# Performance work log

Measured on AMD Instinct MI355X. Metric: run time of the kernel, lower is better.

Reference implementation:

```python
import jax, jax.numpy as jnp
import numpy as np

D_MODEL = 1024
HEADS = 16
D_K = D_MODEL // HEADS

def setup_inputs() -> dict:
    key = jax.random.key(0)
    ks = jax.random.split(key, 12)
    B, S = 4, 2048
    sc = 1.0 / np.sqrt(D_MODEL)
    inp = {
        'q': jax.random.normal(ks[0], (B, S, D_MODEL), jnp.float32),
        'k': jax.random.normal(ks[1], (B, S, D_MODEL), jnp.float32),
        'v': jax.random.normal(ks[2], (B, S, D_MODEL), jnp.float32),
        'mask': jnp.ones((B, S, S), jnp.int32),
        'Wq': jax.random.normal(ks[3], (D_MODEL, D_MODEL), jnp.float32) * sc,
        'bq': jnp.zeros((D_MODEL,), jnp.float32),
        'Wk': jax.random.normal(ks[4], (D_MODEL, D_MODEL), jnp.float32) * sc,
        'bk': jnp.zeros((D_MODEL,), jnp.float32),
        'Wv': jax.random.normal(ks[5], (D_MODEL, D_MODEL), jnp.float32) * sc,
        'bv': jnp.zeros((D_MODEL,), jnp.float32),
        'Wo': jax.random.normal(ks[6], (D_MODEL, D_MODEL), jnp.float32) * sc,
        'bo': jnp.zeros((D_MODEL,), jnp.float32),
    }
    return inp

def _proj_heads(x, W, b):
    # torch Linear: y = x @ W.T + b; then view(B,S,h,dk).transpose(1,2) -> [B,h,S,dk]
    B, S, _ = x.shape
    y = jnp.einsum('bsd,ed->bse', x, W) + b
    return y.reshape(B, S, HEADS, D_K).transpose(0, 2, 1, 3)

def reference(q, k, v, mask, Wq, bq, Wk, bk, Wv, bv, Wo, bo):
    B, S, _ = q.shape
    qh = _proj_heads(q, Wq, bq)  # [B,h,S,dk]
    kh = _proj_heads(k, Wk, bk)
    vh = _proj_heads(v, Wv, bv)
    scores = jnp.einsum('bhqd,bhkd->bhqk', qh, kh) / np.sqrt(D_K)
    scores = jnp.where(mask[:, None, :, :] == 0, jnp.float32(-1e9), scores)
    probs = jax.nn.softmax(scores, axis=-1)  # dropout = identity (eval mode)
    ctx = jnp.einsum('bhqk,bhkd->bhqd', probs, vh)
    concat = ctx.transpose(0, 2, 1, 3).reshape(B, S, D_MODEL)
    return jnp.einsum('bsd,ed->bse', concat, Wo) + bo
```

## Files before the change

### kernel.cpp

```cpp
#include <hip/hip_runtime.h>
#include <stdint.h>

#define DM 1024
#define SQL 2048
#define NB 4
#define NH 16
#define DK 64

typedef unsigned short u16;
typedef unsigned int u32;
typedef float f32x4 __attribute__((ext_vector_type(4)));
typedef short s16x8 __attribute__((ext_vector_type(8)));

__device__ __forceinline__ u16 f2bf(float x) {
  union { float f; u32 u; } un; un.f = x;
  u32 r = un.u + 0x7fffu + ((un.u >> 16) & 1u);
  return (u16)(r >> 16);
}
__device__ __forceinline__ u32 pack_bf16(float a, float b) {
  return (u32)f2bf(a) | ((u32)f2bf(b) << 16);
}

typedef __attribute__((address_space(3))) u32 lds_u32_t;
typedef __attribute__((address_space(1))) u32 g_u32_t;

__device__ __forceinline__ void async_cp16(void* lds, const void* g) {
  __builtin_amdgcn_global_load_lds((g_u32_t*)(unsigned long long)g,
                                   (lds_u32_t*)(unsigned long long)lds,
                                   16, 0, 0);
}

__device__ __forceinline__ void mfma16(f32x4& c, s16x8 a, s16x8 b) {
  c = __builtin_amdgcn_mfma_f32_16x16x32_bf16(a, b, c, 0, 0, 0);
}

__global__ void init_flag_k(int* flag) { if (threadIdx.x == 0) *flag = 1; }

__device__ __forceinline__ void store_bf4(u16* dst, float4 v) {
  u32 lo = pack_bf16(v.x, v.y);
  u32 hi = pack_bf16(v.z, v.w);
  ((u32*)dst)[0] = lo; ((u32*)dst)[1] = hi;
}

__global__ void __launch_bounds__(256) convert_scan_k(
    const float* __restrict__ q, const float* __restrict__ k, const float* __restrict__ v,
    const float* __restrict__ wq, const float* __restrict__ wk,
    const float* __restrict__ wv, const float* __restrict__ wo,
    const int* __restrict__ mask,
    u16* qb, u16* kb, u16* vb, u16* wqb, u16* wkb, u16* wvb, u16* wob, int* flag)
{
  const size_t i = (size_t)blockIdx.x * 256 + threadIdx.x;
  const size_t i4 = i * 4;
  store_bf4(qb + i4, *(const float4*)(q + i4));
  store_bf4(kb + i4, *(const float4*)(k + i4));
  store_bf4(vb + i4, *(const float4*)(v + i4));
  if (i4 < 1048576) {
    store_bf4(wqb + i4, *(const float4*)(wq + i4));
    store_bf4(wkb + i4, *(const float4*)(wk + i4));
    store_bf4(wvb + i4, *(const float4*)(wv + i4));
    store_bf4(wob + i4, *(const float4*)(wo + i4));
  }
  const size_t mi = i * 8;
  int4 m0 = *(const int4*)(mask + mi);
  int4 m1 = *(const int4*)(mask + mi + 4);
  bool z = (m0.x == 0) | (m0.y == 0) | (m0.z == 0) | (m0.w == 0) |
           (m1.x == 0) | (m1.y == 0) | (m1.z == 0) | (m1.w == 0);
  if (z) *flag = 0;
}

__device__ __forceinline__ void gemm_core(const u16* __restrict__ A, const u16* __restrict__ W,
                                          int m0, int n0, u16* sA, u16* sB, f32x4 (&acc)[4][4])
{
  const int tid = threadIdx.x;
  const int l = tid & 63, w = tid >> 6;
  const int g = l >> 4, ln = l & 15;
  const int wm = w & 1, wn = w >> 1;

  for (int kt = 0; kt < DM; kt += 64) {
#pragma unroll
    for (int i = 0; i < 4; ++i) {
      int s = w * 256 + i * 64 + l;
      int m = s >> 3;
      int kc = (s & 7) ^ (m & 7);
      async_cp16(sA + (size_t)(w * 256 + i * 64) * 8,
                 A + (size_t)(m0 + m) * DM + kt + kc * 8);
    }
#pragma unroll
    for (int i = 0; i < 4; ++i) {
      int s = w * 256 + i * 64 + l;
      int n = s >> 3;
      int kc = (s & 7) ^ (n & 7);
      async_cp16(sB + (size_t)(w * 256 + i * 64) * 8,
                 W + (size_t)(n0 + n) * DM + kt + kc * 8);
    }
    asm volatile("s_waitcnt vmcnt(0)" ::: "memory");
    __syncthreads();
#pragma unroll
    for (int ks = 0; ks < 2; ++ks) {
      s16x8 af[4], bfr[4];
#pragma unroll
      for (int mt = 0; mt < 4; ++mt) {
        int m = wm * 64 + mt * 16 + ln;
        int slot = m * 8 + ((ks * 4 + g) ^ (m & 7));
        af[mt] = *(const s16x8*)(sA + (size_t)slot * 8);
      }
#pragma unroll
      for (int nt = 0; nt < 4; ++nt) {
        int n = wn * 64 + nt * 16 + ln;
        int slot = n * 8 + ((ks * 4 + g) ^ (n & 7));
        bfr[nt] = *(const s16x8*)(sB + (size_t)slot * 8);
      }
#pragma unroll
      for (int mt = 0; mt < 4; ++mt)
#pragma unroll
        for (int nt = 0; nt < 4; ++nt)
          mfma16(acc[mt][nt], af[mt], bfr[nt]);
    }
    __syncthreads();
  }
}

__global__ void __launch_bounds__(256) gemm_qkv_k(
    const u16* __restrict__ qb, const u16* __restrict__ kb, const u16* __restrict__ vb,
    const u16* __restrict__ wqb, const u16* __restrict__ wkb, const u16* __restrict__ wvb,
    const float* __restrict__ bq, const float* __restrict__ bk, const float* __restrict__ bv,
    u16* Qh, u16* Kh, u16* Vt)
{
  __shared__ __align__(16) u16 sA[128 * 64];
  __shared__ __align__(16) u16 sB[128 * 64];
  const int z = blockIdx.z;
  const u16* A = (z == 0) ? qb : ((z == 1) ? kb : vb);
  const u16* W = (z == 0) ? wqb : ((z == 1) ? wkb : wvb);
  const float* bias = (z == 0) ? bq : ((z == 1) ? bk : bv);
  const int m0 = blockIdx.y * 128, n0 = blockIdx.x * 128;

  f32x4 zero4 = {0.f, 0.f, 0.f, 0.f};
  f32x4 acc[4][4];
#pragma unroll
  for (int mt = 0; mt < 4; ++mt)
#pragma unroll
    for (int nt = 0; nt < 4; ++nt) acc[mt][nt] = zero4;

  gemm_core(A, W, m0, n0, sA, sB, acc);

  const int tid = threadIdx.x;
  const int l = tid & 63, w = tid >> 6, g = l >> 4, ln = l & 15;
  const int wm = w & 1, wn = w >> 1;
  const float scale = (z == 0) ? (0.125f * 1.44269504089f) : 1.0f;
  u16* Crow = (z == 0) ? Qh : Kh;
#pragma unroll
  for (int nt = 0; nt < 4; ++nt) {
    int n = n0 + wn * 64 + nt * 16 + ln;
    float bn = bias[n];
#pragma unroll
    for (int mt = 0; mt < 4; ++mt) {
      int mb = m0 + wm * 64 + mt * 16 + g * 4;
      f32x4 vv = acc[mt][nt];
      if (z < 2) {
#pragma unroll
        for (int r = 0; r < 4; ++r)
          Crow[(size_t)(mb + r) * DM + n] = f2bf((vv[r] + bn) * scale);
      } else {
        int b = mb >> 11, s = mb & 2047;
        u32 lo = pack_bf16(vv[0] + bn, vv[1] + bn);
        u32 hi = pack_bf16(vv[2] + bn, vv[3] + bn);
        u32* dst = (u32*)(Vt + ((size_t)b << 21) + (size_t)n * SQL + s);
        dst[0] = lo; dst[1] = hi;
      }
    }
  }
}

__global__ void __launch_bounds__(256, 4) attn_k(
    const u16* __restrict__ Qh, const u16* __restrict__ Kh, const u16* __restrict__ Vt,
    const int* __restrict__ mask, const int* __restrict__ flag, u16* __restrict__ ctx)
{
  __shared__ __align__(16) u16 smem[16384];
  u16* Ks = smem;
  u16* Vs = smem + 8192;
  const int tid = threadIdx.x;
  const int l = tid & 63, w = tid >> 6, g = l >> 4, ln = l & 15;
  const int wq = w >> 1, wk = w & 1;
  const int q0 = blockIdx.x * 64;
  const int h = blockIdx.y, b = blockIdx.z;
  const int allones = *flag;

  s16x8 qf[2][2];
#pragma unroll
  for (int u = 0; u < 2; ++u)
#pragma unroll
    for (int ks = 0; ks < 2; ++ks) {
      size_t row = (size_t)(b * SQL + q0 + wq * 32 + u * 16 + ln);
      qf[u][ks] = *(const s16x8*)(Qh + row * DM + h * DK + ks * 32 + g * 8);
    }

  f32x4 zero4 = {0.f, 0.f, 0.f, 0.f};
  f32x4 ot[4][2];
#pragma unroll
  for (int mt = 0; mt < 4; ++mt) { ot[mt][0] = zero4; ot[mt][1] = zero4; }
  float lsum[2] = {0.f, 0.f};

  const int LA = (g & 1) * 32 + ln;
  const int LB = LA + 16;
  const bool ghi = (g >> 1) != 0;

  for (int kv0 = 0; kv0 < SQL; kv0 += 128) {
#pragma unroll
    for (int i = 0; i < 4; ++i) {
      int s = w * 256 + i * 64 + l;
      int m = s >> 3;
      int kc = (s & 7) ^ (m & 7);
      async_cp16(Ks + (size_t)(w * 256 + i * 64) * 8,
                 Kh + (size_t)(b * SQL + kv0 + m) * DM + h * DK + kc * 8);
    }
#pragma unroll
    for (int i = 0; i < 4; ++i) {
      int s = w * 256 + i * 64 + l;
      int d = s >> 4;
      int kc = (s & 15) ^ (d & 15);
      async_cp16(Vs + (size_t)(w * 256 + i * 64) * 8,
                 Vt + ((size_t)b << 21) + (size_t)(h * DK + d) * SQL + kv0 + kc * 8);
    }
    asm volatile("s_waitcnt vmcnt(0)" ::: "memory");
    __syncthreads();

    f32x4 st[4][2];
#pragma unroll
    for (int t = 0; t < 4; ++t) { st[t][0] = zero4; st[t][1] = zero4; }
#pragma unroll
    for (int ks = 0; ks < 2; ++ks) {
#pragma unroll
      for (int t = 0; t < 4; ++t) {
        int m = wk * 64 + t * 16 + ln;
        int slot = m * 8 + ((ks * 4 + g) ^ (m & 7));
        s16x8 kf = *(const s16x8*)(Ks + (size_t)slot * 8);
        mfma16(st[t][0], kf, qf[0][ks]);
        mfma16(st[t][1], kf, qf[1][ks]);
      }
    }

    if (!allones) {
      const int* mb_ = mask + (size_t)b * SQL * SQL;
#pragma unroll
      for (int t = 0; t < 4; ++t)
#pragma unroll
        for (int u = 0; u < 2; ++u)
#pragma unroll
          for (int r = 0; r < 4; ++r) {
            int kv = kv0 + wk * 64 + t * 16 + g * 4 + r;
            int qq = q0 + wq * 32 + u * 16 + ln;
            if (mb_[(size_t)qq * SQL + kv] == 0) st[t][u][r] = -30.f;
          }
    }

    u32 pk[2][4][2];
#pragma unroll
    for (int u = 0; u < 2; ++u) {
      float rs = 0.f;
#pragma unroll
      for (int t = 0; t < 4; ++t) {
        float p0 = __builtin_amdgcn_exp2f(st[t][u][0]);
        float p1 = __builtin_amdgcn_exp2f(st[t][u][1]);
        float p2 = __builtin_amdgcn_exp2f(st[t][u][2]);
        float p3 = __builtin_amdgcn_exp2f(st[t][u][3]);
        rs += (p0 + p1) + (p2 + p3);
        pk[u][t][0] = pack_bf16(p0, p1);
        pk[u][t][1] = pack_bf16(p2, p3);
      }
      rs += __shfl_xor(rs, 16, 64);
      rs += __shfl_xor(rs, 32, 64);
      lsum[u] += rs;
    }

#pragma unroll
    for (int kc = 0; kc < 2; ++kc) {
      s16x8 pf[2];
#pragma unroll
      for (int u = 0; u < 2; ++u) {
        u32 a0 = __shfl(pk[u][kc * 2][0], LA, 64);
        u32 a1 = __shfl(pk[u][kc * 2][1], LA, 64);
        u32 b0 = __shfl(pk[u][kc * 2][0], LB, 64);
        u32 b1 = __shfl(pk[u][kc * 2][1], LB, 64);
        u32 c0 = __shfl(pk[u][kc * 2 + 1][0], LA, 64);
        u32 c1 = __shfl(pk[u][kc * 2 + 1][1], LA, 64);
        u32 d0 = __shfl(pk[u][kc * 2 + 1][0], LB, 64);
        u32 d1 = __shfl(pk[u][kc * 2 + 1][1], LB, 64);
        union { u32 wds[4]; s16x8 v; } pu;
        pu.wds[0] = ghi ? c0 : a0;
        pu.wds[1] = ghi ? c1 : a1;
        pu.wds[2] = ghi ? d0 : b0;
        pu.wds[3] = ghi ? d1 : b1;
        pf[u] = pu.v;
      }
#pragma unroll
      for (int mt = 0; mt < 4; ++mt) {
        int d = mt * 16 + ln;
        int slot = d * 16 + ((wk * 8 + kc * 4 + g) ^ (d & 15));
        s16x8 vf = *(const s16x8*)(Vs + (size_t)slot * 8);
        mfma16(ot[mt][0], vf, pf[0]);
        mfma16(ot[mt][1], vf, pf[1]);
      }
    }
    __syncthreads();
  }

  float* red = (float*)smem;
  if (wk == 1) {
#pragma unroll
    for (int u = 0; u < 2; ++u) {
      int row = wq * 32 + u * 16 + ln;
#pragma unroll
      for (int mt = 0; mt < 4; ++mt)
        *(f32x4*)&red[(size_t)row * 68 + mt * 16 + g * 4] = ot[mt][u];
      if (g == 0) red[(size_t)row * 68 + 64] = lsum[u];
    }
  }
  __syncthreads();
  if (wk == 0) {
#pragma unroll
    for (int u = 0; u < 2; ++u) {
      int row = wq * 32 + u * 16 + ln;
#pragma unroll
      for (int mt = 0; mt < 4; ++mt)
        ot[mt][u] += *(const f32x4*)&red[(size_t)row * 68 + mt * 16 + g * 4];
      lsum[u] += red[(size_t)row * 68 + 64];
    }
#pragma unroll
    for (int u = 0; u < 2; ++u) {
      float inv = 1.0f / lsum[u];
      size_t row = (size_t)(b * SQL + q0 + wq * 32 + u * 16 + ln);
#pragma unroll
      for (int mt = 0; mt < 4; ++mt) {
        u32 lo = pack_bf16(ot[mt][u][0] * inv, ot[mt][u][1] * inv);
        u32 hi = pack_bf16(ot[mt][u][2] * inv, ot[mt][u][3] * inv);
        u32* dst = (u32*)(ctx + row * DM + h * DK + mt * 16 + g * 4);
        dst[0] = lo; dst[1] = hi;
      }
    }
  }
}

__global__ void __launch_bounds__(256) gemm_out_k(
    const u16* __restrict__ ctx, const u16* __restrict__ wob,
    const float* __restrict__ bo, float* __restrict__ out)
{
  __shared__ __align__(16) u16 sA[128 * 64];
  __shared__ __align__(16) u16 sB[128 * 64];
  const int m0 = blockIdx.y * 128, n0 = blockIdx.x * 128;
  f32x4 zero4 = {0.f, 0.f, 0.f, 0.f};
  f32x4 acc[4][4];
#pragma unroll
  for (int mt = 0; mt < 4; ++mt)
#pragma unroll
    for (int nt = 0; nt < 4; ++nt) acc[mt][nt] = zero4;

  gemm_core(ctx, wob, m0, n0, sA, sB, acc);

  const int tid = threadIdx.x;
  const int l = tid & 63, w = tid >> 6, g = l >> 4, ln = l & 15;
  const int wm = w & 1, wn = w >> 1;
#pragma unroll
  for (int nt = 0; nt < 4; ++nt) {
    int n = n0 + wn * 64 + nt * 16 + ln;
    float bn = bo[n];
#pragma unroll
    for (int mt = 0; mt < 4; ++mt) {
      int mb = m0 + wm * 64 + mt * 16 + g * 4;
      f32x4 vv = acc[mt][nt];
#pragma unroll
      for (int r = 0; r < 4; ++r)
        out[(size_t)(mb + r) * DM + n] = vv[r] + bn;
    }
  }
}

extern "C" void kernel_launch(void* const* d_in, const int* in_sizes, int n_in,
                              void* d_out, int out_size, void* d_ws, size_t ws_size,
                              hipStream_t stream) {
  (void)in_sizes; (void)n_in; (void)out_size; (void)ws_size;
  const float* q  = (const float*)d_in[0];
  const float* k  = (const float*)d_in[1];
  const float* v  = (const float*)d_in[2];
  const int* mask = (const int*)d_in[3];
  const float* Wq = (const float*)d_in[4];
  const float* bq = (const float*)d_in[5];
  const float* Wk = (const float*)d_in[6];
  const float* bk = (const float*)d_in[7];
  const float* Wv = (const float*)d_in[8];
  const float* bv = (const float*)d_in[9];
  const float* Wo = (const float*)d_in[10];
  const float* bo = (const float*)d_in[11];
  float* out = (float*)d_out;
  char* ws = (char*)d_ws;

  u16* qb  = (u16*)(ws + 0);
  u16* kb  = (u16*)(ws + 16777216);
  u16* vb  = (u16*)(ws + 33554432);
  u16* Qh  = (u16*)(ws + 50331648);
  u16* Kh  = (u16*)(ws + 67108864);
  u16* Vt  = (u16*)(ws + 83886080);
  u16* ctx = (u16*)(ws + 100663296);
  u16* wqb = (u16*)(ws + 117440512);
  u16* wkb = (u16*)(ws + 119537664);
  u16* wvb = (u16*)(ws + 121634816);
  u16* wob = (u16*)(ws + 123731968);
  int* flag = (int*)(ws + 125829120);

  hipLaunchKernelGGL(init_flag_k, dim3(1), dim3(64), 0, stream, flag);
  hipLaunchKernelGGL(convert_scan_k, dim3(8192), dim3(256), 0, stream,
                     q, k, v, Wq, Wk, Wv, Wo, mask,
                     qb, kb, vb, wqb, wkb, wvb, wob, flag);
  hipLaunchKernelGGL(gemm_qkv_k, dim3(8, 64, 3), dim3(256), 0, stream,
                     qb, kb, vb, wqb, wkb, wvb, bq, bk, bv, Qh, Kh, Vt);
  hipLaunchKernelGGL(attn_k, dim3(32, 16, 4), dim3(256), 0, stream,
                     Qh, Kh, Vt, mask, flag, ctx);
  hipLaunchKernelGGL(gemm_out_k, dim3(8, 64), dim3(256), 0, stream,
                     ctx, wob, bo, out);
}
```

Baseline: 472.3 us.

## Double-buffer K/V staging in attention and remap blocks for locality

The attention kernel now prefetches the next 128-key K/V tile into a second LDS buffer while computing the current one, waiting with partial vmcnt and raw s_barrier. Block indices are remapped so that neighbouring blocks spread across batch/head groups, the row-sum shuffle reduction moves out of the loop, and the epilogue stages normalized output through LDS for coalesced bf16 stores. bf16 rounding is simplified from round-to-nearest-even to round-half-up. LDS doubles and the occupancy hint drops from 4 to 2 blocks, trading occupancy for overlap of loads and compute.

```diff
diff --git a/kernel.cpp b/kernel.cpp
--- a/kernel.cpp
+++ b/kernel.cpp
@@ -14,8 +14,7 @@
 
 __device__ __forceinline__ u16 f2bf(float x) {
   union { float f; u32 u; } un; un.f = x;
-  u32 r = un.u + 0x7fffu + ((un.u >> 16) & 1u);
-  return (u16)(r >> 16);
+  return (u16)((un.u + 0x8000u) >> 16);
 }
 __device__ __forceinline__ u32 pack_bf16(float a, float b) {
   return (u32)f2bf(a) | ((u32)f2bf(b) << 16);
@@ -171,18 +170,41 @@
   }
 }
 
-__global__ void __launch_bounds__(256, 4) attn_k(
+__device__ __forceinline__ void stage_kv(u16* Ks, u16* Vs,
+                                         const u16* __restrict__ Kh,
+                                         const u16* __restrict__ Vt,
+                                         int b, int h, int kv0, int w, int l) {
+#pragma unroll
+  for (int i = 0; i < 4; ++i) {
+    int s = w * 256 + i * 64 + l;
+    int m = s >> 3;
+    int kc = (s & 7) ^ (m & 7);
+    async_cp16(Ks + (size_t)(w * 256 + i * 64) * 8,
+               Kh + (size_t)(b * SQL + kv0 + m) * DM + h * DK + kc * 8);
+  }
+#pragma unroll
+  for (int i = 0; i < 4; ++i) {
+    int s = w * 256 + i * 64 + l;
+    int d = s >> 4;
+    int kc = (s & 15) ^ (d & 15);
+    async_cp16(Vs + (size_t)(w * 256 + i * 64) * 8,
+               Vt + ((size_t)b << 21) + (size_t)(h * DK + d) * SQL + kv0 + kc * 8);
+  }
+}
+
+__global__ void __launch_bounds__(256, 2) attn_k(
     const u16* __restrict__ Qh, const u16* __restrict__ Kh, const u16* __restrict__ Vt,
     const int* __restrict__ mask, const int* __restrict__ flag, u16* __restrict__ ctx)
 {
-  __shared__ __align__(16) u16 smem[16384];
-  u16* Ks = smem;
-  u16* Vs = smem + 8192;
+  __shared__ __align__(16) u16 smem[32768];
   const int tid = threadIdx.x;
   const int l = tid & 63, w = tid >> 6, g = l >> 4, ln = l & 15;
   const int wq = w >> 1, wk = w & 1;
-  const int q0 = blockIdx.x * 64;
-  const int h = blockIdx.y, b = blockIdx.z;
+  const int flat = blockIdx.x + 32 * (blockIdx.y + 16 * blockIdx.z);
+  const int nid = (flat & 7) * 256 + (flat >> 3);
+  const int q0 = (nid & 31) * 64;
+  const int bh = nid >> 5;
+  const int h = bh & 15, b = bh >> 4;
   const int allones = *flag;
 
   s16x8 qf[2][2];
@@ -204,72 +226,63 @@
   const int LB = LA + 16;
   const bool ghi = (g >> 1) != 0;
 
-  for (int kv0 = 0; kv0 < SQL; kv0 += 128) {
-#pragma unroll
-    for (int i = 0; i < 4; ++i) {
-      int s = w * 256 + i * 64 + l;
-      int m = s >> 3;
-      int kc = (s & 7) ^ (m & 7);
-      async_cp16(Ks + (size_t)(w * 256 + i * 64) * 8,
-                 Kh + (size_t)(b * SQL + kv0 + m) * DM + h * DK + kc * 8);
-    }
-#pragma unroll
-    for (int i = 0; i < 4; ++i) {
-      int s = w * 256 + i * 64 + l;
-      int d = s >> 4;
-      int kc = (s & 15) ^ (d & 15);
-      async_cp16(Vs + (size_t)(w * 256 + i * 64) * 8,
-                 Vt + ((size_t)b << 21) + (size_t)(h * DK + d) * SQL + kv0 + kc * 8);
-    }
-    asm volatile("s_waitcnt vmcnt(0)" ::: "memory");
-    __syncthreads();
+  stage_kv(smem, smem + 8192, Kh, Vt, b, h, 0, w, l);
+
+  for (int t = 0; t < 16; ++t) {
+    const int kv0 = t * 128;
+    u16* Ks = smem + (t & 1) * 16384;
+    u16* Vs = smem + 8192 + (t & 1) * 16384;
+    if (t < 15) {
+      stage_kv(smem + ((t + 1) & 1) * 16384, smem + 8192 + ((t + 1) & 1) * 16384,
+               Kh, Vt, b, h, kv0 + 128, w, l);
+      asm volatile("s_waitcnt vmcnt(8)" ::: "memory");
+    } else {
+      asm volatile("s_waitcnt vmcnt(0)" ::: "memory");
+    }
+    asm volatile("s_barrier" ::: "memory");
 
     f32x4 st[4][2];
 #pragma unroll
-    for (int t = 0; t < 4; ++t) { st[t][0] = zero4; st[t][1] = zero4; }
+    for (int t2 = 0; t2 < 4; ++t2) { st[t2][0] = zero4; st[t2][1] = zero4; }
 #pragma unroll
     for (int ks = 0; ks < 2; ++ks) {
 #pragma unroll
-      for (int t = 0; t < 4; ++t) {
-        int m = wk * 64 + t * 16 + ln;
+      for (int t2 = 0; t2 < 4; ++t2) {
+        int m = wk * 64 + t2 * 16 + ln;
         int slot = m * 8 + ((ks * 4 + g) ^ (m & 7));
         s16x8 kf = *(const s16x8*)(Ks + (size_t)slot * 8);
-        mfma16(st[t][0], kf, qf[0][ks]);
-        mfma16(st[t][1], kf, qf[1][ks]);
+        mfma16(st[t2][0], kf, qf[0][ks]);
+        mfma16(st[t2][1], kf, qf[1][ks]);
       }
     }
 
     if (!allones) {
       const int* mb_ = mask + (size_t)b * SQL * SQL;
 #pragma unroll
-      for (int t = 0; t < 4; ++t)
+      for (int t2 = 0; t2 < 4; ++t2)
 #pragma unroll
         for (int u = 0; u < 2; ++u)
 #pragma unroll
           for (int r = 0; r < 4; ++r) {
-            int kv = kv0 + wk * 64 + t * 16 + g * 4 + r;
+            int kv = kv0 + wk * 64 + t2 * 16 + g * 4 + r;
             int qq = q0 + wq * 32 + u * 16 + ln;
-            if (mb_[(size_t)qq * SQL + kv] == 0) st[t][u][r] = -30.f;
+            if (mb_[(size_t)qq * SQL + kv] == 0) st[t2][u][r] = -30.f;
           }
     }
 
     u32 pk[2][4][2];
 #pragma unroll
     for (int u = 0; u < 2; ++u) {
-      float rs = 0.f;
-#pragma unroll
-      for (int t = 0; t < 4; ++t) {
-        float p0 = __builtin_amdgcn_exp2f(st[t][u][0]);
-        float p1 = __builtin_amdgcn_exp2f(st[t][u][1]);
-        float p2 = __builtin_amdgcn_exp2f(st[t][u][2]);
-        float p3 = __builtin_amdgcn_exp2f(st[t][u][3]);
-        rs += (p0 + p1) + (p2 + p3);
-        pk[u][t][0] = pack_bf16(p0, p1);
-        pk[u][t][1] = pack_bf16(p2, p3);
-      }
-      rs += __shfl_xor(rs, 16, 64);
-      rs += __shfl_xor(rs, 32, 64);
-      lsum[u] += rs;
+#pragma unroll
+      for (int t2 = 0; t2 < 4; ++t2) {
+        float p0 = __builtin_amdgcn_exp2f(st[t2][u][0]);
+        float p1 = __builtin_amdgcn_exp2f(st[t2][u][1]);
+        float p2 = __builtin_amdgcn_exp2f(st[t2][u][2]);
+        float p3 = __builtin_amdgcn_exp2f(st[t2][u][3]);
+        lsum[u] += (p0 + p1) + (p2 + p3);
+        pk[u][t2][0] = pack_bf16(p0, p1);
+        pk[u][t2][1] = pack_bf16(p2, p3);
+      }
     }
 
 #pragma unroll
@@ -301,10 +314,19 @@
         mfma16(ot[mt][1], vf, pf[1]);
       }
     }
-    __syncthreads();
+
+    asm volatile("s_waitcnt lgkmcnt(0)" ::: "memory");
+    asm volatile("s_barrier" ::: "memory");
+  }
+
+#pragma unroll
+  for (int u = 0; u < 2; ++u) {
+    lsum[u] += __shfl_xor(lsum[u], 16, 64);
+    lsum[u] += __shfl_xor(lsum[u], 32, 64);
   }
 
   float* red = (float*)smem;
+  __syncthreads();
   if (wk == 1) {
 #pragma unroll
     for (int u = 0; u < 2; ++u) {
@@ -325,18 +347,28 @@
         ot[mt][u] += *(const f32x4*)&red[(size_t)row * 68 + mt * 16 + g * 4];
       lsum[u] += red[(size_t)row * 68 + 64];
     }
+  }
+  __syncthreads();
+  if (wk == 0) {
 #pragma unroll
     for (int u = 0; u < 2; ++u) {
       float inv = 1.0f / lsum[u];
-      size_t row = (size_t)(b * SQL + q0 + wq * 32 + u * 16 + ln);
-#pragma unroll
-      for (int mt = 0; mt < 4; ++mt) {
-        u32 lo = pack_bf16(ot[mt][u][0] * inv, ot[mt][u][1] * inv);
-        u32 hi = pack_bf16(ot[mt][u][2] * inv, ot[mt][u][3] * inv);
-        u32* dst = (u32*)(ctx + row * DM + h * DK + mt * 16 + g * 4);
-        dst[0] = lo; dst[1] = hi;
-      }
-    }
+      int row = wq * 32 + u * 16 + ln;
+#pragma unroll
+      for (int mt = 0; mt < 4; ++mt)
+#pragma unroll
+        for (int r = 0; r < 4; ++r)
+          red[(size_t)row * 68 + mt * 16 + g * 4 + r] = ot[mt][u][r] * inv;
+    }
+  }
+  __syncthreads();
+#pragma unroll
+  for (int i = 0; i < 8; ++i) {
+    int f2 = i * 256 + tid;
+    int qq = f2 >> 5, dp = f2 & 31;
+    float2 vv = *(const float2*)&red[(size_t)qq * 68 + dp * 2];
+    u32 pkd = pack_bf16(vv.x, vv.y);
+    *(u32*)(ctx + (size_t)(b * SQL + q0 + qq) * DM + h * DK + dp * 2) = pkd;
   }
 }
 
```

Measured after the change: 455.1 us. -3.6%, faster.
